# Performance work log

Hardware: AMD Instinct MI355X
Metric: run time of the kernel (lower is better)

The kernel has to match this reference:

```python
import jax, jax.numpy as jnp
import numpy as np


def setup_inputs() -> dict:
    key = jax.random.key(0)
    k1, k2 = jax.random.split(key)
    B, N, M, C = 32, 4096, 4096, 3
    xyz1 = jax.random.normal(k1, (B, N, C), dtype=jnp.float32)
    xyz2 = jax.random.normal(k2, (B, M, C), dtype=jnp.float32)
    return {"xyz1": xyz1, "xyz2": xyz2}


def _chamfer_l2(xyz1, xyz2):
    # Pairwise squared L2 distances via ||a||^2 + ||b||^2 - 2 a.b  (b n m)
    sq1 = jnp.sum(xyz1 * xyz1, axis=-1)            # [B, N]
    sq2 = jnp.sum(xyz2 * xyz2, axis=-1)            # [B, M]
    cross = jnp.einsum('bnc,bmc->bnm', xyz1, xyz2) # [B, N, M]
    d = sq1[:, :, None] + sq2[:, None, :] - 2.0 * cross
    dist1 = jnp.min(d, axis=2)                     # [B, N] nearest in xyz2
    dist2 = jnp.min(d, axis=1)                     # [B, M] nearest in xyz1
    return jnp.mean(dist1, axis=-1) + jnp.mean(dist2, axis=-1)  # [B]


def reference(xyz1, xyz2):
    return _chamfer_l2(xyz1, xyz2)
```

## Files before the change

kernel.cpp:

```cpp
#include <hip/hip_runtime.h>

typedef _Float16 half8 __attribute__((ext_vector_type(8)));
typedef float floatx16 __attribute__((ext_vector_type(16)));

#define TPB    256
#define RPTS   256
#define NTILE  (RPTS / 32)
#define SMH    (RPTS * 16)
#define NSPLIT 4


__device__ __forceinline__ void wr_point(_Float16* __restrict__ smb, int j,
                                         float x, float y, float z) {
    float hq = 0.5f * (x * x + y * y + z * z);
    _Float16 xh = (_Float16)x, yh = (_Float16)y, zh = (_Float16)z;
    _Float16 xl = (_Float16)(x - (float)xh);
    _Float16 yl = (_Float16)(y - (float)yh);
    _Float16 zl = (_Float16)(z - (float)zh);
    _Float16 qh = (_Float16)hq;
    _Float16 ql = (_Float16)(hq - (float)qh);
    const _Float16 hz = (_Float16)0.0f;
    int t = j >> 5, c = j & 31;
    half8 v0, v1;
    v0[0] = xh; v0[1] = xl; v0[2] = xh; v0[3] = yh;
    v0[4] = yl; v0[5] = yh; v0[6] = zh; v0[7] = zl;
    v1[0] = zh; v1[1] = qh; v1[2] = ql; v1[3] = hz;
    v1[4] = hz; v1[5] = hz; v1[6] = hz; v1[7] = hz;
    *(half8*)&smb[t * 512 + c * 8]       = v0;
    *(half8*)&smb[t * 512 + 256 + c * 8] = v1;
}

__device__ __forceinline__ float fold16(floatx16 d) {
    float m0 = fminf(fminf(d[0],  d[1]),  d[2]);
    float m1 = fminf(fminf(d[3],  d[4]),  d[5]);
    float m2 = fminf(fminf(d[6],  d[7]),  d[8]);
    float m3 = fminf(fminf(d[9],  d[10]), d[11]);
    float m4 = fminf(fminf(d[12], d[13]), d[14]);
    float n0 = fminf(fminf(m0, m1), m2);
    float n1 = fminf(fminf(m3, m4), d[15]);
    return fminf(n0, n1);
}

__global__ __launch_bounds__(TPB, 4) void chamfer_mfma(const float* __restrict__ xyz1,
                                                       const float* __restrict__ xyz2,
                                                       float* __restrict__ ws,
                                                       int N, int M, int QCAP) {
    const int b = blockIdx.y, dir = blockIdx.z;
    const int B = gridDim.y;
    const int qblock = (int)blockIdx.x / NSPLIT;
    const int chunk  = (int)blockIdx.x % NSPLIT;
    const float* __restrict__ P = dir ? xyz2 + (size_t)b * M * 3 : xyz1 + (size_t)b * N * 3;
    const float* __restrict__ Q = dir ? xyz1 + (size_t)b * N * 3 : xyz2 + (size_t)b * M * 3;
    const int nq = dir ? M : N;
    const int md = dir ? N : M;

    if (qblock * 256 >= nq) return;

    const int CH   = ((md + NSPLIT * RPTS - 1) / (NSPLIT * RPTS)) * RPTS;
    const int base = chunk * CH;
    const int nrounds = CH / RPTS;

    __shared__ __align__(16) _Float16 smB[2][SMH];

    const int tid = (int)threadIdx.x;
    const int w   = tid >> 6;
    const int l   = tid & 63;
    const int m   = l & 31;
    const int h   = l >> 5;

    const _Float16 hz = (_Float16)0.0f, hone = (_Float16)1.0f;
    const int qb = qblock * 256 + w * 64;

    half8 qfr[2];
#pragma unroll
    for (int g = 0; g < 2; ++g) {
        int idx = qb + g * 32 + m;
        int ci  = idx < nq ? idx : nq - 1;
        float x = P[3 * ci], y = P[3 * ci + 1], z = P[3 * ci + 2];
        _Float16 xh = (_Float16)x, yh = (_Float16)y, zh = (_Float16)z;
        _Float16 xl = (_Float16)(x - (float)xh);
        _Float16 yl = (_Float16)(y - (float)yh);
        _Float16 zl = (_Float16)(z - (float)zh);
        half8 a;
        if (h == 0) {
            a[0] = -xh; a[1] = -xh; a[2] = -xl; a[3] = -yh;
            a[4] = -yh; a[5] = -yl; a[6] = -zh; a[7] = -zh;
        } else {
            a[0] = -zl; a[1] = hone; a[2] = hone; a[3] = hz;
            a[4] = hz;  a[5] = hz;   a[6] = hz;  a[7] = hz;
        }
        qfr[g] = a;
    }

    float sx0, sy0, sz0;
#define LDPTS(rr) {                                                   \
        int g0 = base + (rr) * RPTS + tid;                            \
        g0 = g0 < md ? g0 : md - 1;   \
        sx0 = Q[3 * g0]; sy0 = Q[3 * g0 + 1]; sz0 = Q[3 * g0 + 2];    \
    }
#define WRPTS(bb) { wr_point(&smB[bb][0], tid, sx0, sy0, sz0); }

    float rmq0 = 3.0e38f, rmq1 = 3.0e38f;

    const floatx16 czero = {0.0f, 0.0f, 0.0f, 0.0f, 0.0f, 0.0f, 0.0f, 0.0f,
                            0.0f, 0.0f, 0.0f, 0.0f, 0.0f, 0.0f, 0.0f, 0.0f};

    LDPTS(0);
    WRPTS(0);
    if (nrounds > 1) LDPTS(1);
    __syncthreads();

    const _Float16* bp0 = &smB[0][h * 256 + m * 8];
    const _Float16* bp1 = &smB[1][h * 256 + m * 8];

    int cur = 0;
    for (int r = 0; r < nrounds; ++r) {
        if (r + 1 < nrounds) {
            WRPTS(cur ^ 1);
            if (r + 2 < nrounds) LDPTS(r + 2);
        }

        const _Float16* bp = cur ? bp1 : bp0;
#pragma unroll 1
        for (int t = 0; t < NTILE; t += 2) {
            half8 a0 = *(const half8*)(bp + t * 512);
            half8 a1 = *(const half8*)(bp + t * 512 + 512);
            floatx16 d;
            d = __builtin_amdgcn_mfma_f32_32x32x16_f16(a0, qfr[0], czero, 0, 0, 0);
            rmq0 = fminf(rmq0, fold16(d));
            d = __builtin_amdgcn_mfma_f32_32x32x16_f16(a0, qfr[1], czero, 0, 0, 0);
            rmq1 = fminf(rmq1, fold16(d));
            d = __builtin_amdgcn_mfma_f32_32x32x16_f16(a1, qfr[0], czero, 0, 0, 0);
            rmq0 = fminf(rmq0, fold16(d));
            d = __builtin_amdgcn_mfma_f32_32x32x16_f16(a1, qfr[1], czero, 0, 0, 0);
            rmq1 = fminf(rmq1, fold16(d));
        }

        if (r + 1 < nrounds) __syncthreads();
        cur ^= 1;
    }

    rmq0 = fminf(rmq0, __shfl_xor(rmq0, 32, 64));
    rmq1 = fminf(rmq1, __shfl_xor(rmq1, 32, 64));

    float* __restrict__ wsd = ws + (((size_t)chunk * 2 + dir) * B + b) * QCAP;
    const int idx = qb + l;
    const float val = h ? rmq1 : rmq0;
    if (idx < nq) wsd[idx] = val;
}

__global__ __launch_bounds__(256) void chamfer_reduce(const float* __restrict__ xyz1,
                                                      const float* __restrict__ xyz2,
                                                      const float* __restrict__ ws,
                                                      float* __restrict__ out,
                                                      int N, int M, int QCAP) {
    const int b = (int)blockIdx.x, dir = (int)blockIdx.y;
    const int B = gridDim.x;
    const float* __restrict__ P = dir ? xyz2 + (size_t)b * M * 3 : xyz1 + (size_t)b * N * 3;
    const int nq = dir ? M : N;
    const size_t cs = (size_t)2 * B * QCAP;
    const float* __restrict__ w0 = ws + ((size_t)dir * B + b) * QCAP;

    float s = 0.0f;
    for (int q = (int)threadIdx.x + (int)blockIdx.z * 256; q < nq; q += 256 * (int)gridDim.z) {
        float v = w0[q];
#pragma unroll
        for (int c = 1; c < NSPLIT; ++c) v = fminf(v, w0[c * cs + q]);
        float x = P[3 * q], y = P[3 * q + 1], z = P[3 * q + 2];
        s += v + 0.5f * (x * x + y * y + z * z);
    }
#pragma unroll
    for (int off = 32; off > 0; off >>= 1) s += __shfl_down(s, off, 64);
    __shared__ float red[4];
    if ((threadIdx.x & 63) == 0) red[threadIdx.x >> 6] = s;
    __syncthreads();
    if (threadIdx.x == 0) {
        float t = (red[0] + red[1]) + (red[2] + red[3]);
        atomicAdd(out + b, t * (2.0f / (float)nq));
    }
}

extern "C" void kernel_launch(void* const* d_in, const int* in_sizes, int n_in,
                              void* d_out, int out_size, void* d_ws, size_t ws_size,
                              hipStream_t stream) {
    const float* xyz1 = (const float*)d_in[0];
    const float* xyz2 = (const float*)d_in[1];
    float* out = (float*)d_out;

    const int B = out_size;
    const int N = in_sizes[0] / (3 * B);
    const int M = in_sizes[1] / (3 * B);

    hipMemsetAsync(d_out, 0, (size_t)B * sizeof(float), stream);

    const int qmax    = N > M ? N : M;
    const int qblocks = (qmax + 255) / 256;
    const int QCAP    = qblocks * 256;

    dim3 grid(qblocks * NSPLIT, B, 2);
    chamfer_mfma<<<grid, dim3(TPB), 0, stream>>>(xyz1, xyz2, (float*)d_ws, N, M, QCAP);
    chamfer_reduce<<<dim3(B, 2, 4), dim3(256), 0, stream>>>(xyz1, xyz2, (float*)d_ws, out, N, M, QCAP);
}
```

Measured before the change: 97.78 us.

## Stage whole 1024-point chunk once and register-prefetch tiles from LDS

The multi-round double-buffered shared-memory pipeline is replaced by a single up-front load of one 1024-point chunk into LDS, followed by one barrier, so the inner loop has no per-round syncs. The MMA loop now prefetches the next pair of half8 fragments into registers while the current ones are consumed. The number of chunks is now computed from the problem size rather than fixed, giving 4 chunks for 4096 points, the same split as before. It trades load/compute overlap across rounds for fewer barriers and a simpler loop. The loaded global points are all exposed before compute starts.

```diff
diff --git a/kernel.cpp b/kernel.cpp
--- a/kernel.cpp
+++ b/kernel.cpp
@@ -4,11 +4,21 @@
 typedef float floatx16 __attribute__((ext_vector_type(16)));
 
 #define TPB    256
-#define RPTS   256
-#define NTILE  (RPTS / 32)
-#define SMH    (RPTS * 16)
-#define NSPLIT 4
-
+#define CHUNK  1024
+#define NTILE  (CHUNK / 32)
+#define SMH    (CHUNK * 16)
+
+
+__device__ __forceinline__ float fold16(floatx16 d) {
+    float m0 = fminf(fminf(d[0],  d[1]),  d[2]);
+    float m1 = fminf(fminf(d[3],  d[4]),  d[5]);
+    float m2 = fminf(fminf(d[6],  d[7]),  d[8]);
+    float m3 = fminf(fminf(d[9],  d[10]), d[11]);
+    float m4 = fminf(fminf(d[12], d[13]), d[14]);
+    float n0 = fminf(fminf(m0, m1), m2);
+    float n1 = fminf(fminf(m3, m4), d[15]);
+    return fminf(n0, n1);
+}
 
 __device__ __forceinline__ void wr_point(_Float16* __restrict__ smb, int j,
                                          float x, float y, float z) {
@@ -30,25 +40,15 @@
     *(half8*)&smb[t * 512 + 256 + c * 8] = v1;
 }
 
-__device__ __forceinline__ float fold16(floatx16 d) {
-    float m0 = fminf(fminf(d[0],  d[1]),  d[2]);
-    float m1 = fminf(fminf(d[3],  d[4]),  d[5]);
-    float m2 = fminf(fminf(d[6],  d[7]),  d[8]);
-    float m3 = fminf(fminf(d[9],  d[10]), d[11]);
-    float m4 = fminf(fminf(d[12], d[13]), d[14]);
-    float n0 = fminf(fminf(m0, m1), m2);
-    float n1 = fminf(fminf(m3, m4), d[15]);
-    return fminf(n0, n1);
-}
-
 __global__ __launch_bounds__(TPB, 4) void chamfer_mfma(const float* __restrict__ xyz1,
                                                        const float* __restrict__ xyz2,
                                                        float* __restrict__ ws,
-                                                       int N, int M, int QCAP) {
+                                                       int N, int M, int QCAP,
+                                                       int nchunks) {
     const int b = blockIdx.y, dir = blockIdx.z;
     const int B = gridDim.y;
-    const int qblock = (int)blockIdx.x / NSPLIT;
-    const int chunk  = (int)blockIdx.x % NSPLIT;
+    const int qblock = (int)blockIdx.x / nchunks;
+    const int chunk  = (int)blockIdx.x % nchunks;
     const float* __restrict__ P = dir ? xyz2 + (size_t)b * M * 3 : xyz1 + (size_t)b * N * 3;
     const float* __restrict__ Q = dir ? xyz1 + (size_t)b * N * 3 : xyz2 + (size_t)b * M * 3;
     const int nq = dir ? M : N;
@@ -56,11 +56,9 @@
 
     if (qblock * 256 >= nq) return;
 
-    const int CH   = ((md + NSPLIT * RPTS - 1) / (NSPLIT * RPTS)) * RPTS;
-    const int base = chunk * CH;
-    const int nrounds = CH / RPTS;
-
-    __shared__ __align__(16) _Float16 smB[2][SMH];
+    const int base = chunk * CHUNK;
+
+    __shared__ __align__(16) _Float16 smB[SMH];
 
     const int tid = (int)threadIdx.x;
     const int w   = tid >> 6;
@@ -92,52 +90,49 @@
         qfr[g] = a;
     }
 
-    float sx0, sy0, sz0;
-#define LDPTS(rr) {                                                   \
-        int g0 = base + (rr) * RPTS + tid;                            \
-        g0 = g0 < md ? g0 : md - 1;   \
-        sx0 = Q[3 * g0]; sy0 = Q[3 * g0 + 1]; sz0 = Q[3 * g0 + 2];    \
-    }
-#define WRPTS(bb) { wr_point(&smB[bb][0], tid, sx0, sy0, sz0); }
+    {
+        int g0 = base + tid;
+        int g1 = base + tid + 256;
+        int g2 = base + tid + 512;
+        int g3 = base + tid + 768;
+        g0 = g0 < md ? g0 : md - 1;
+        g1 = g1 < md ? g1 : md - 1;
+        g2 = g2 < md ? g2 : md - 1;
+        g3 = g3 < md ? g3 : md - 1;
+        float x0 = Q[3 * g0], y0 = Q[3 * g0 + 1], z0 = Q[3 * g0 + 2];
+        float x1 = Q[3 * g1], y1 = Q[3 * g1 + 1], z1 = Q[3 * g1 + 2];
+        float x2 = Q[3 * g2], y2 = Q[3 * g2 + 1], z2 = Q[3 * g2 + 2];
+        float x3 = Q[3 * g3], y3 = Q[3 * g3 + 1], z3 = Q[3 * g3 + 2];
+        wr_point(smB, tid,       x0, y0, z0);
+        wr_point(smB, tid + 256, x1, y1, z1);
+        wr_point(smB, tid + 512, x2, y2, z2);
+        wr_point(smB, tid + 768, x3, y3, z3);
+    }
+    __syncthreads();
 
     float rmq0 = 3.0e38f, rmq1 = 3.0e38f;
 
     const floatx16 czero = {0.0f, 0.0f, 0.0f, 0.0f, 0.0f, 0.0f, 0.0f, 0.0f,
                             0.0f, 0.0f, 0.0f, 0.0f, 0.0f, 0.0f, 0.0f, 0.0f};
 
-    LDPTS(0);
-    WRPTS(0);
-    if (nrounds > 1) LDPTS(1);
-    __syncthreads();
-
-    const _Float16* bp0 = &smB[0][h * 256 + m * 8];
-    const _Float16* bp1 = &smB[1][h * 256 + m * 8];
-
-    int cur = 0;
-    for (int r = 0; r < nrounds; ++r) {
-        if (r + 1 < nrounds) {
-            WRPTS(cur ^ 1);
-            if (r + 2 < nrounds) LDPTS(r + 2);
-        }
-
-        const _Float16* bp = cur ? bp1 : bp0;
+    const _Float16* bp = &smB[h * 256 + m * 8];
+    half8 c0 = *(const half8*)(bp);
+    half8 c1 = *(const half8*)(bp + 512);
 #pragma unroll 1
-        for (int t = 0; t < NTILE; t += 2) {
-            half8 a0 = *(const half8*)(bp + t * 512);
-            half8 a1 = *(const half8*)(bp + t * 512 + 512);
-            floatx16 d;
-            d = __builtin_amdgcn_mfma_f32_32x32x16_f16(a0, qfr[0], czero, 0, 0, 0);
-            rmq0 = fminf(rmq0, fold16(d));
-            d = __builtin_amdgcn_mfma_f32_32x32x16_f16(a0, qfr[1], czero, 0, 0, 0);
-            rmq1 = fminf(rmq1, fold16(d));
-            d = __builtin_amdgcn_mfma_f32_32x32x16_f16(a1, qfr[0], czero, 0, 0, 0);
-            rmq0 = fminf(rmq0, fold16(d));
-            d = __builtin_amdgcn_mfma_f32_32x32x16_f16(a1, qfr[1], czero, 0, 0, 0);
-            rmq1 = fminf(rmq1, fold16(d));
-        }
-
-        if (r + 1 < nrounds) __syncthreads();
-        cur ^= 1;
+    for (int t = 0; t < NTILE; t += 2) {
+        const int t2 = (t + 2) & (NTILE - 1);
+        half8 n0 = *(const half8*)(bp + t2 * 512);
+        half8 n1 = *(const half8*)(bp + t2 * 512 + 512);
+        floatx16 d;
+        d = __builtin_amdgcn_mfma_f32_32x32x16_f16(c0, qfr[0], czero, 0, 0, 0);
+        rmq0 = fminf(rmq0, fold16(d));
+        d = __builtin_amdgcn_mfma_f32_32x32x16_f16(c0, qfr[1], czero, 0, 0, 0);
+        rmq1 = fminf(rmq1, fold16(d));
+        d = __builtin_amdgcn_mfma_f32_32x32x16_f16(c1, qfr[0], czero, 0, 0, 0);
+        rmq0 = fminf(rmq0, fold16(d));
+        d = __builtin_amdgcn_mfma_f32_32x32x16_f16(c1, qfr[1], czero, 0, 0, 0);
+        rmq1 = fminf(rmq1, fold16(d));
+        c0 = n0; c1 = n1;
     }
 
     rmq0 = fminf(rmq0, __shfl_xor(rmq0, 32, 64));
@@ -153,7 +148,8 @@
                                                       const float* __restrict__ xyz2,
                                                       const float* __restrict__ ws,
                                                       float* __restrict__ out,
-                                                      int N, int M, int QCAP) {
+                                                      int N, int M, int QCAP,
+                                                      int nchunks) {
     const int b = (int)blockIdx.x, dir = (int)blockIdx.y;
     const int B = gridDim.x;
     const float* __restrict__ P = dir ? xyz2 + (size_t)b * M * 3 : xyz1 + (size_t)b * N * 3;
@@ -164,8 +160,7 @@
     float s = 0.0f;
     for (int q = (int)threadIdx.x + (int)blockIdx.z * 256; q < nq; q += 256 * (int)gridDim.z) {
         float v = w0[q];
-#pragma unroll
-        for (int c = 1; c < NSPLIT; ++c) v = fminf(v, w0[c * cs + q]);
+        for (int c = 1; c < nchunks; ++c) v = fminf(v, w0[c * cs + q]);
         float x = P[3 * q], y = P[3 * q + 1], z = P[3 * q + 2];
         s += v + 0.5f * (x * x + y * y + z * z);
     }
@@ -196,8 +191,10 @@
     const int qmax    = N > M ? N : M;
     const int qblocks = (qmax + 255) / 256;
     const int QCAP    = qblocks * 256;
-
-    dim3 grid(qblocks * NSPLIT, B, 2);
-    chamfer_mfma<<<grid, dim3(TPB), 0, stream>>>(xyz1, xyz2, (float*)d_ws, N, M, QCAP);
-    chamfer_reduce<<<dim3(B, 2, 4), dim3(256), 0, stream>>>(xyz1, xyz2, (float*)d_ws, out, N, M, QCAP);
-}
+    const int mdmax   = qmax;
+    const int nchunks = (mdmax + CHUNK - 1) / CHUNK;
+
+    dim3 grid(qblocks * nchunks, B, 2);
+    chamfer_mfma<<<grid, dim3(TPB), 0, stream>>>(xyz1, xyz2, (float*)d_ws, N, M, QCAP, nchunks);
+    chamfer_reduce<<<dim3(B, 2, 4), dim3(256), 0, stream>>>(xyz1, xyz2, (float*)d_ws, out, N, M, QCAP, nchunks);
+}
```

After: 101.1 us. 3.4% more time.
